# Kernel tuning notes

Measured on AMD Instinct MI355X. Metric: run time of the kernel, lower is better.

Reference implementation:

```python
import jax, jax.numpy as jnp
import numpy as np
from math import factorial

# ---------------- real Wigner-3j coefficients (l <= 2) ----------------

def _w3j_c(l1, l2, l3, m1, m2, m3):
    if m1 + m2 + m3 != 0:
        return 0.0
    f = factorial
    pref = ((-1.0) ** (l1 - l2 - m3)) * np.sqrt(
        f(l1 + l2 - l3) * f(l1 - l2 + l3) * f(-l1 + l2 + l3) / f(l1 + l2 + l3 + 1)
        * f(l1 + m1) * f(l1 - m1) * f(l2 + m2) * f(l2 - m2) * f(l3 + m3) * f(l3 - m3))
    s = 0.0
    for t in range(0, l1 + l2 - l3 + 1):
        ds = [t, l3 - l2 + t + m1, l3 - l1 + t - m2, l1 + l2 - l3 - t, l1 - t - m1, l2 - t + m2]
        if min(ds) < 0:
            continue
        den = 1
        for d in ds:
            den *= f(d)
        s += ((-1.0) ** t) / den
    return pref * s

def _u_real(l):
    # complex->real spherical-harmonic change of basis (rows: mu=-l..l, cols: m=-l..l)
    U = np.zeros((2 * l + 1, 2 * l + 1), dtype=np.complex128)
    U[l, l] = 1.0
    for m in range(1, l + 1):
        U[l + m, l + m] = ((-1) ** m) / np.sqrt(2)
        U[l + m, l - m] = 1.0 / np.sqrt(2)
        U[l - m, l - m] = 1j / np.sqrt(2)
        U[l - m, l + m] = -1j * ((-1) ** m) / np.sqrt(2)
    return U

def _real_w3j(l1, l2, l3):
    W = np.zeros((2 * l1 + 1, 2 * l2 + 1, 2 * l3 + 1), dtype=np.complex128)
    for a, m1 in enumerate(range(-l1, l1 + 1)):
        for b, m2 in enumerate(range(-l2, l2 + 1)):
            for c, m3 in enumerate(range(-l3, l3 + 1)):
                W[a, b, c] = _w3j_c(l1, l2, l3, m1, m2, m3)
    C = np.einsum('am,bn,co,mno->abc', _u_real(l1), _u_real(l2), _u_real(l3), W)
    C = C.real + C.imag  # each entry is purely real or purely imaginary
    n = np.linalg.norm(C)
    if n > 0:
        C = C / n
    return jnp.asarray(C, dtype=jnp.float32)

W3J = {(l1, l2, l3): _real_w3j(l1, l2, l3)
       for l1 in range(3) for l2 in range(3) for l3 in range(3)
       if abs(l1 - l2) <= l3 <= l1 + l2}

SH_OFF = [0, 1, 4]
RELU_GAIN = float(np.sqrt(2.0))  # normalize2mom gain for ReLU

# ---------------- building blocks ----------------

def tp_instructions(in_ls):
    # input irrep blocks have parity (-1)**l (0e,1o,2e); sh = 0e+1o+2e; out = 0e+1o+2e
    ins = []
    for i1, l1 in enumerate(in_ls):
        for l2 in range(3):
            for l3 in range(3):
                if abs(l1 - l2) <= l3 <= l1 + l2 and ((-1) ** (l1 + l2)) == (-1) ** l3:
                    ins.append((i1, l1, l2, l3))
    return ins

def sh_l2(d):
    # component-normalized real spherical harmonics of unit vectors, l=0..2
    x, y, z = d[:, 0], d[:, 1], d[:, 2]
    s3, s15, s5 = np.sqrt(3.0), np.sqrt(15.0), np.sqrt(5.0)
    sh0 = jnp.ones_like(x)[:, None]
    sh1 = jnp.stack([s3 * y, s3 * z, s3 * x], axis=1)
    sh2 = jnp.stack([s15 * x * y, s15 * y * z, (s5 / 2) * (3 * z * z - 1.0),
                     s15 * x * z, (s15 / 2) * (x * x - y * y)], axis=1)
    return jnp.concatenate([sh0, sh1, sh2], axis=1)

def radial_basis(d, num=11, start=0.0, end=8.0):
    values = jnp.linspace(start, end, num)
    step = values[1] - values[0]
    diff = (d[:, None] - values) / step
    return jnp.exp(-(diff * diff)) / 1.12  # e3nn soft_one_hot_linspace 'gaussian'

def radial_net(rb, w1, w2):
    h = jax.nn.relu(rb @ (w1 / np.sqrt(w1.shape[0]))) * RELU_GAIN
    return h @ (w2 / np.sqrt(w2.shape[0]))

def equiv_conv(pos, x, src, dst, rw1, rw2, in_ls, mul_in, C):
    E = src.shape[0]
    vec = pos[src] - pos[dst]                      # (E,3)
    dist = jnp.sqrt(jnp.sum(vec * vec, axis=1))    # (E,)
    w = radial_net(radial_basis(dist), rw1, rw2)   # (E, weight_numel)
    dirs = vec / jnp.maximum(dist, 1e-12)[:, None]
    sh = sh_l2(dirs)                               # (E,9)
    xd = x[dst]                                    # edge gather
    ins = tp_instructions(in_ls)
    fan = {0: 0, 1: 0, 2: 0}
    for (_, l1, l2, l3) in ins:
        fan[l3] += mul_in
    in_off = np.cumsum([0] + [mul_in * (2 * l + 1) for l in in_ls])
    out = [jnp.zeros((E, C, 2 * l3 + 1), x.dtype) for l3 in range(3)]
    woff = 0
    for (i1, l1, l2, l3) in ins:
        x1 = xd[:, in_off[i1]:in_off[i1 + 1]].reshape(E, mul_in, 2 * l1 + 1)
        shb = sh[:, SH_OFF[l2]:SH_OFF[l2] + 2 * l2 + 1]
        wi = w[:, woff:woff + mul_in * C].reshape(E, mul_in, C)
        woff += mul_in * C
        alpha = np.sqrt(2 * l3 + 1) / np.sqrt(fan[l3])
        out[l3] = out[l3] + alpha * jnp.einsum('eui,ej,euw,ijk->ewk', x1, shb, wi, W3J[(l1, l2, l3)])
    msg = jnp.concatenate([o.reshape(E, -1) for o in out], axis=1)
    return jax.ops.segment_sum(msg, src, num_segments=pos.shape[0])  # scatter_add onto src

def self_interaction(x, W, mul_in):
    # x: mul_in x (0e+1o+2e); W: (3, mul_in, mul_out)
    outs, off = [], 0
    for l in range(3):
        d = 2 * l + 1
        b = x[:, off:off + mul_in * d].reshape(-1, mul_in, d)
        off += mul_in * d
        outs.append((jnp.einsum('nui,uw->nwi', b, W[l]) / np.sqrt(mul_in)).reshape(x.shape[0], -1))
    return jnp.concatenate(outs, axis=1)

def pointwise_nonlin(x, b, mul):
    outs, off = [], 0
    for l in range(3):
        d = 2 * l + 1
        blk = x[:, off:off + mul * d]
        off += mul * d
        if l == 0:
            outs.append(jax.nn.softplus(blk + b[0]))
        else:
            v = blk.reshape(-1, mul, d)
            gate = jax.nn.softplus(jnp.sqrt(jnp.sum(v * v, axis=2) + 1e-24) + b[l])
            outs.append((v * gate[:, :, None]).reshape(x.shape[0], -1))
    return jnp.concatenate(outs, axis=1)

def pointwise_norm(x):
    return x / (jnp.linalg.norm(x, axis=1, keepdims=True) + 1e-6)

def backbone(pos, features, edge_index, si0_w, c1_rw1, c1_rw2, si1_w, nl1_b,
             c2_rw1, c2_rw2, si2_w, nl2_b, c3_rw1, c3_rw2, si3_w, nl3_b, fsi_w):
    src, dst = edge_index[0], edge_index[1]
    x = features @ si0_w / np.sqrt(features.shape[1])          # 64x0e -> 128x0e
    x = equiv_conv(pos, x, src, dst, c1_rw1, c1_rw2, [0], 128, 128)
    x = pointwise_norm(x)
    x = self_interaction(x, si1_w, 128)
    x = pointwise_nonlin(x, nl1_b, 128)
    x = equiv_conv(pos, x, src, dst, c2_rw1, c2_rw2, [0, 1, 2], 128, 64)
    x = pointwise_norm(x)
    x = self_interaction(x, si2_w, 64)
    x = pointwise_nonlin(x, nl2_b, 64)
    x = equiv_conv(pos, x, src, dst, c3_rw1, c3_rw2, [0, 1, 2], 64, 32)
    x = pointwise_norm(x)
    x = self_interaction(x, si3_w, 32)
    x = pointwise_nonlin(x, nl3_b, 32)
    x = self_interaction(x, fsi_w, 32)
    return x[:, :32]  # scalar (0e) part

# ---------------- harness ----------------

N_NODES, N_EDGES, FEAT = 512, 2048, 64

def setup_inputs() -> dict:
    key = jax.random.key(0)
    ks = jax.random.split(key, 20)
    src = jax.random.randint(ks[0], (N_EDGES,), 0, N_NODES)
    # avoid self-loops (zero-length edges are degenerate for normalize/grad)
    dst = (src + 1 + jax.random.randint(ks[1], (N_EDGES,), 0, N_NODES - 1)) % N_NODES
    edge_index = jnp.stack([src, dst]).astype(jnp.int64)
    rn = lambda k, s: jax.random.normal(k, s, dtype=jnp.float32)
    return {
        'pos': rn(ks[2], (N_NODES, 3)),
        'features': rn(ks[3], (N_NODES, FEAT)),
        'edge_index': edge_index,
        'si0_w': rn(ks[4], (FEAT, 128)),
        'c1_rw1': rn(ks[5], (11, 12)), 'c1_rw2': rn(ks[6], (12, 3 * 128 * 128)),
        'si1_w': rn(ks[7], (3, 128, 128)), 'nl1_b': jnp.zeros((3,), jnp.float32),
        'c2_rw1': rn(ks[8], (11, 12)), 'c2_rw2': rn(ks[9], (12, 11 * 128 * 64)),
        'si2_w': rn(ks[10], (3, 64, 64)), 'nl2_b': jnp.zeros((3,), jnp.float32),
        'c3_rw1': rn(ks[11], (11, 12)), 'c3_rw2': rn(ks[12], (12, 11 * 64 * 32)),
        'si3_w': rn(ks[13], (3, 32, 32)), 'nl3_b': jnp.zeros((3,), jnp.float32),
        'fsi_w': rn(ks[14], (3, 32, 32)),
    }

def reference(pos, features, edge_index, si0_w, c1_rw1, c1_rw2, si1_w, nl1_b,
              c2_rw1, c2_rw2, si2_w, nl2_b, c3_rw1, c3_rw2, si3_w, nl3_b, fsi_w):
    return backbone(pos, features, edge_index, si0_w, c1_rw1, c1_rw2, si1_w, nl1_b,
                    c2_rw1, c2_rw2, si2_w, nl2_b, c3_rw1, c3_rw2, si3_w, nl3_b, fsi_w)
```

## Files before the change

kernel.cpp:

```cpp
#include <hip/hip_runtime.h>
#include <cmath>
#include <cstdint>

#define NNODES 512
#define NEDGES 2048

typedef _Float16 half2v __attribute__((ext_vector_type(2)));

#define OFF_W3J   0
#define OFF_SH    512
#define OFF_H1    (OFF_SH + NEDGES*9)
#define OFF_H2    (OFF_H1 + NEDGES*6)
#define OFF_H3    (OFF_H2 + NEDGES*6)
#define OFF_W2P1  (OFF_H3 + NEDGES*6)
#define OFF_W2P2  (OFF_W2P1 + 6*49152)
#define OFF_W2P3  (OFF_W2P2 + 6*90112)
#define OFF_XH    (OFF_W2P3 + 6*22528)
#define OFF_XB    (OFF_XH + NNODES*576)
#define OFF_MSGA  (OFF_XB + NNODES*1152)
#define OFF_CNT   (OFF_MSGA + NEDGES*576)
#define OFF_COFF  (OFF_CNT + 512)
#define OFF_LIST  (OFF_COFF + 1024)
#define OFF_RANK  (OFF_LIST + 2048)
#define OFF_MSGB  (OFF_RANK + 2048)
#define WS_NEED_SPLIT ((size_t)(OFF_MSGB + NEDGES*576) * 4)

__device__ __forceinline__ unsigned int packh2f(float a, float b){
  half2v h; h.x=(_Float16)a; h.y=(_Float16)b;
  return __builtin_bit_cast(unsigned int, h);
}
__device__ __forceinline__ half2v u2h2(unsigned int u){ return __builtin_bit_cast(half2v, u); }
__device__ __forceinline__ float dot2f(unsigned int a, unsigned int b, float c){
#if __has_builtin(__builtin_amdgcn_fdot2)
  return __builtin_amdgcn_fdot2(u2h2(a), u2h2(b), c, false);
#else
  half2v ha=u2h2(a), hb=u2h2(b);
  return c + (float)ha.x*(float)hb.x + (float)ha.y*(float)hb.y;
#endif
}
__device__ __forceinline__ unsigned int pk2(float a, float b){
#if __has_builtin(__builtin_amdgcn_cvt_pkrtz)
  auto h=__builtin_amdgcn_cvt_pkrtz(a,b);
  return __builtin_bit_cast(unsigned int,h);
#else
  return packh2f(a,b);
#endif
}
__device__ __forceinline__ unsigned short f2h(float f){
  _Float16 h=(_Float16)f; return __builtin_bit_cast(unsigned short,h);
}
__device__ __forceinline__ float softplusf(float v){ return fmaxf(v,0.f)+log1pf(expf(-fabsf(v))); }

__device__ double dfact(int n){ double f=1.0; for(int i=2;i<=n;++i) f*=(double)i; return f; }

__device__ double w3j_c_dev(int l1,int l2,int l3,int m1,int m2,int m3){
  if (m1+m2+m3 != 0) return 0.0;
  int p = l1 - l2 - m3;
  double sign = (((p%2)+2)%2) ? -1.0 : 1.0;
  double pref = sign*sqrt(dfact(l1+l2-l3)*dfact(l1-l2+l3)*dfact(-l1+l2+l3)/dfact(l1+l2+l3+1)
              *dfact(l1+m1)*dfact(l1-m1)*dfact(l2+m2)*dfact(l2-m2)*dfact(l3+m3)*dfact(l3-m3));
  double s=0.0;
  for (int t=0;t<=l1+l2-l3;++t){
    int d0=t, d1v=l3-l2+t+m1, d2v=l3-l1+t-m2, d3v=l1+l2-l3-t, d4=l1-t-m1, d5=l2-t+m2;
    if (d0<0||d1v<0||d2v<0||d3v<0||d4<0||d5<0) continue;
    double den=dfact(d0)*dfact(d1v)*dfact(d2v)*dfact(d3v)*dfact(d4)*dfact(d5);
    s += ((t&1)?-1.0:1.0)/den;
  }
  return pref*s;
}

__device__ void u_real_dev(int l, double Ur[5][5], double Ui[5][5]){
  for(int a=0;a<5;++a)for(int b=0;b<5;++b){Ur[a][b]=0.0;Ui[a][b]=0.0;}
  Ur[l][l]=1.0;
  double inv2 = 1.0/sqrt(2.0);
  for(int m=1;m<=l;++m){
    double sgn = (m&1)?-1.0:1.0;
    Ur[l+m][l+m] = sgn*inv2;
    Ur[l+m][l-m] = inv2;
    Ui[l-m][l-m] = inv2;
    Ui[l-m][l+m] = -sgn*inv2;
  }
}

__global__ void w3j_kernel(float* __restrict__ out){
  const int L1[11]={0,0,0,1,1,1,1,2,2,2,2};
  const int L2[11]={0,1,2,0,1,1,2,0,1,2,2};
  const int L3[11]={0,1,2,1,0,2,1,2,1,0,2};
  const int OFF[11]={0,1,10,35,44,53,98,143,168,213,238};
  int t = blockIdx.x;
  int tid = threadIdx.x;
  int l1=L1[t], l2=L2[t], l3=L3[t];
  int d1=2*l1+1, d2=2*l2+1, d3=2*l3+1;
  int sz=d1*d2*d3;
  __shared__ double Wt[125];
  __shared__ double U1r[5][5],U1i[5][5],U2r[5][5],U2i[5][5],U3r[5][5],U3i[5][5];
  __shared__ double Cv[125];
  __shared__ double red[128];
  for(int idx=tid; idx<sz; idx+=128){
    int a=idx/(d2*d3), rem=idx%(d2*d3), b=rem/d3, c=rem%d3;
    Wt[idx]=w3j_c_dev(l1,l2,l3,a-l1,b-l2,c-l3);
  }
  if(tid==0) u_real_dev(l1,U1r,U1i);
  if(tid==1) u_real_dev(l2,U2r,U2i);
  if(tid==2) u_real_dev(l3,U3r,U3i);
  __syncthreads();
  for(int idx=tid; idx<sz; idx+=128){
    int a=idx/(d2*d3), rem=idx%(d2*d3), b=rem/d3, c=rem%d3;
    double cr=0.0, ci=0.0;
    for(int m=0;m<d1;++m)for(int n=0;n<d2;++n){
// ... 124 lines not shown
  int i=col>>7, w=col&127;
  int d3=2*i+1;
  float alpha=sqrtf((float)(2*i+1))*(1.f/sqrtf(128.f));
  int e0=blockIdx.x*2;
  #pragma unroll
  for(int s=0;s<2;++s){
    int e=e0+s;
    int n=dstp[e];
    const unsigned int* vp=V+((size_t)n*384+col)*6;
    float G=0.f;
    #pragma unroll
    for(int r2=0;r2<6;++r2) G=dot2f(h1[(size_t)e*6+r2], vp[r2], G);
    int base=(i==0)?0:((i==1)?128:512);
    for(int k=0;k<d3;++k){
      float B=0.f;
      for(int j=0;j<d3;++j) B += shb[(size_t)e*9+i*i+j]*w3j[W3O[i]+j*d3+k];
      m16[(size_t)e*1152 + base + w*d3 + k]=f2h(G*B*alpha);
    }
  }
}

__global__ __launch_bounds__(256) void csr_rank_kernel(const int* __restrict__ src,
    int* __restrict__ cnt, int* __restrict__ rankA){
  __shared__ int s_src[NEDGES];
  int tid=threadIdx.x;
  int4* s4=(int4*)s_src;
  const int4* g4=(const int4*)src;
  for(int i=tid;i<NEDGES/4;i+=256) s4[i]=g4[i];
  __syncthreads();
  int e=blockIdx.x*256+tid;
  int s=s_src[e];
  int lt=0, tot=0;
  for(int b=0;b<NEDGES/4;b+=8){
    int4 v[8];
    #pragma unroll
    for(int k=0;k<8;++k) v[k]=s4[b+k];
    #pragma unroll
    for(int k=0;k<8;++k){
      int j0=4*(b+k);
      tot += ((v[k].x==s)?1:0)+((v[k].y==s)?1:0)+((v[k].z==s)?1:0)+((v[k].w==s)?1:0);
      lt  += ((v[k].x==s&&j0<e)?1:0)+((v[k].y==s&&j0+1<e)?1:0)+((v[k].z==s&&j0+2<e)?1:0)+((v[k].w==s&&j0+3<e)?1:0);
    }
  }
  rankA[e]=lt;
  if(lt==tot-1) cnt[s]=tot;
}

__global__ void csr_scan_kernel(const int* __restrict__ cnt, int* __restrict__ coff){
  __shared__ int s[NNODES];
  int tid=threadIdx.x;
  s[tid]=cnt[tid];
  __syncthreads();
  for(int d=1;d<NNODES;d<<=1){
    int v=(tid>=d)?s[tid-d]:0;
    __syncthreads();
    s[tid]+=v;
    __syncthreads();
  }
  coff[tid+1]=s[tid];
  if(tid==0) coff[0]=0;
}

__global__ void csr_scatter_kernel(const int* __restrict__ src, const int* __restrict__ coff,
    const int* __restrict__ rankA, int* __restrict__ list){
  int e=blockIdx.x*256+threadIdx.x;
  int s=src[e];
  list[coff[s]+rankA[e]]=e;
}

__global__ void si0_kernel(const float* __restrict__ feat, const float* __restrict__ w,
                           unsigned int* __restrict__ xh){
  __shared__ float s_f[64];
  __shared__ unsigned short s_v[128];
  int n=blockIdx.x, tid=threadIdx.x;
  if(tid<64) s_f[tid]=feat[n*64+tid];
  __syncthreads();
  float acc=0.f;
  for(int u=0;u<64;++u) acc += s_f[u]*w[u*128+tid];
  s_v[tid]=f2h(acc*0.125f);
  __syncthreads();
  if(tid<64) xh[(size_t)n*64+tid]=((unsigned int)s_v[2*tid+1]<<16)|s_v[2*tid];
}

struct CInstr { int l1,l2,l3,woff,w3off; float alpha; };
struct LayerArg { CInstr ins[3][4]; int cnt[3]; int gOf[8]; int rank[8]; int nxg[3]; };

template<int MUL,int C,int EB,int NL,int USPLIT,int D3,int L1v>
__device__ __forceinline__ void instr_body(
  const unsigned int* __restrict__ W2h, int nW, int woff,
  const unsigned int (&hreg)[EB][6],
  const uint4* s_xp4, const float* sB,
  float (&acc)[EB][D3], int ubase, int uOff2, int w)
{
  constexpr int D1=2*L1v+1;
  constexpr int MULZ=MUL/USPLIT;
  constexpr int MZ2=MULZ/2;
  constexpr int UC=256/C;
  constexpr int CHZ=MUL/(UC*USPLIT);
  constexpr int CB=(L1v==0)?0:((L1v==1)?MZ2:4*MZ2);
  static_assert(EB==4,"EB must be 4");
  static_assert(CHZ>=2 && (CHZ&1)==0,"CHZ even");
  const unsigned int* Wp = W2h + (size_t)woff + (size_t)ubase*C + w;
  float a2[EB][D1];
  #pragma unroll
  for(int e=0;e<EB;++e){
    #pragma unroll
    for(int i=0;i<D1;++i) a2[e][i]=0.f;
  }
  #pragma unroll 2
  for(int u2=0;u2<CHZ/2;++u2){
    unsigned int wv0[6],wv1[6];
    #pragma unroll
    for(int r=0;r<6;++r){
      wv0[r]=Wp[(size_t)r*nW + (size_t)(2*u2)*C];
      wv1[r]=Wp[(size_t)r*nW + (size_t)(2*u2+1)*C];
    }
    unsigned int wi2[EB];
    #pragma unroll
    for(int e=0;e<EB;++e){
      float w0=0.f,w1=0.f;
      #pragma unroll
      for(int r=0;r<6;++r){ w0=dot2f(hreg[e][r],wv0[r],w0); w1=dot2f(hreg[e][r],wv1[r],w1); }
      wi2[e]=pk2(w0,w1);
    }
    #pragma unroll
    for(int i=0;i<D1;++i){
      uint4 xv = s_xp4[CB + i*MZ2 + uOff2 + u2];
      a2[0][i]=dot2f(wi2[0],xv.x,a2[0][i]);
      a2[1][i]=dot2f(wi2[1],xv.y,a2[1][i]);
      a2[2][i]=dot2f(wi2[2],xv.z,a2[2][i]);
      a2[3][i]=dot2f(wi2[3],xv.w,a2[3][i]);
    }
  }
  #pragma unroll
  for(int e=0;e<EB;++e){
    #pragma unroll
    for(int k=0;k<D3;++k){
      float s=0.f;
      #pragma unroll
      for(int i=0;i<D1;++i) s += a2[e][i]*sB[e*25+i*5+k];
      acc[e][k]+=s;
    }
  }
}

template<int MUL,int C,int EB,int NL,int USPLIT,int D3,int NINS>
__device__ __forceinline__ void conv_main(
  const unsigned int* __restrict__ W2h, int nW,
  const unsigned int (&hreg)[EB][6],
  const uint4* s_xp4, const float* s_B, float* s_red, unsigned short* s_msg,
  unsigned int* __restrict__ msg, const LayerArg& la, int g, int e0,
  int w, int uc, int ubase, int uOff2)
{
  constexpr int UC=256/C;
  const int tid=threadIdx.x;
  float acc[EB][D3];
  #pragma unroll
  for(int e=0;e<EB;++e){
    #pragma unroll
    for(int k=0;k<D3;++k) acc[e][k]=0.f;
  }
  #pragma unroll
  for(int ii=0;ii<NINS;++ii){
    const int l1v=la.ins[g][ii].l1;
    const int woff=la.ins[g][ii].woff;
    switch(l1v){
      case 0: instr_body<MUL,C,EB,NL,USPLIT,D3,0>(W2h,nW,woff,hreg,s_xp4,s_B+ii*EB*25,acc,ubase,uOff2,w); break;
      case 1: instr_body<MUL,C,EB,NL,USPLIT,D3,1>(W2h,nW,woff,hreg,s_xp4,s_B+ii*EB*25,acc,ubase,uOff2,w); break;
      default: instr_body<MUL,C,EB,NL,USPLIT,D3,2>(W2h,nW,woff,hreg,s_xp4,s_B+ii*EB*25,acc,ubase,uOff2,w); break;
    }
  }
  constexpr int L3v=(D3-1)/2;
  constexpr int base32=(L3v==0)?0:((L3v==1)?C/2:2*C);
  constexpr int seg32=C*D3/2;
  for(int e=0;e<EB;++e){
    #pragma unroll
    for(int k=0;k<D3;++k) s_red[k*256+tid]=acc[e][k];
    __syncthreads();
    if(uc==0){
      #pragma unroll
      for(int k=0;k<D3;++k){
        float s=0.f;
        #pragma unroll
        for(int c2=0;c2<UC;++c2) s+=s_red[k*256+c2*C+w];
        s_msg[(e*C+w)*D3+k]=f2h(s);
      }
    }
    __syncthreads();
  }
  const unsigned int* sm32=(const unsigned int*)s_msg;
  for(int ix=tid; ix<EB*seg32; ix+=256){
    int e=ix/seg32, o=ix-e*seg32;
    msg[(size_t)(e0+e)*(9*C/2) + base32 + o] = sm32[e*seg32+o];
  }
}

template<int MUL,int C,int EB,int NL,int USPLIT>
__global__ __launch_bounds__(256,4) void conv_kernel(
  const unsigned int* __restrict__ xh, const unsigned int* __restrict__ W2h, int nW,
  const unsigned int* __restrict__ hb, const float* __restrict__ shb,
  const int* __restrict__ dstp, const float* __restrict__ w3j,
  unsigned int* __restrict__ msg0, unsigned int* __restrict__ msg1, LayerArg la)
{
  constexpr int MUL2=MUL/2;
  constexpr int MULZ=MUL/USPLIT;
  constexpr int MZ2=MULZ/2;
  constexpr int ROW=(NL==1)?MUL2:9*MUL2;
  constexpr int SROW=(NL==1)?MZ2:9*MZ2;
  constexpr int UC=256/C;
  constexpr int CHZ=MUL/(UC*USPLIT);
  constexpr int NB=NEDGES/EB;
  __shared__ unsigned int s_xp[SROW*EB];
  __shared__ float s_B[4*EB*25];
  __shared__ float s_red[5*256];
  __shared__ unsigned short s_msg[EB*C*5];
  int tid=threadIdx.x;
  int bid=blockIdx.x;
  int xcd=bid&7, slot=bid>>3;
  int g=la.gOf[xcd];
  int idx=slot*la.nxg[g]+la.rank[xcd];
  if(idx>=NB*USPLIT) return;
  int zz=idx/NB, et=idx-zz*NB;
  int e0=et*EB;
  unsigned int* msg=(zz==0)?msg0:msg1;
  for(int ix=tid; ix<EB*SROW; ix+=256){
    int e=ix/SROW, c=ix-(ix/SROW)*SROW;
    int l1,i,u2l;
    if(NL==1){ l1=0;i=0;u2l=c; }
    else{
      if(c<MZ2){l1=0;i=0;u2l=c;}
      else if(c<4*MZ2){int t=c-MZ2;i=t/MZ2;u2l=t-i*MZ2;l1=1;}
      else{int t=c-4*MZ2;i=t/MZ2;u2l=t-i*MZ2;l1=2;}
    }
    int gb=(l1==0)?0:((l1==1)?MUL2:4*MUL2);
    int dn=dstp[e0+e];
    s_xp[c*EB+e]=xh[(size_t)dn*ROW + gb + i*MUL2 + zz*MZ2 + u2l];
  }
  int nIns=la.cnt[g];
  for(int ix=tid; ix<nIns*EB*25; ix+=256){
    int ii=ix/(EB*25); int rem=ix%(EB*25); int e=rem/25; int q=rem%25;
    int i=q/5,k=q%5;
    CInstr I=la.ins[g][ii];
    int d1=2*I.l1+1,d2=2*I.l2+1,d3v=2*I.l3+1;
    float v=0.f;
    if(i<d1&&k<d3v){
      int sho=I.l2*I.l2;
      for(int j=0;j<d2;++j) v+=shb[(size_t)(e0+e)*9+sho+j]*w3j[I.w3off+(i*d2+j)*d3v+k];
      v*=I.alpha;
    }
    s_B[(ii*EB+e)*25+q]=v;
  }
  __syncthreads();
  int w=tid%C, uc=tid/C;
  int ubase=zz*MULZ+uc*CHZ;
  int uOff2=uc*(CHZ/2);
  unsigned int hreg[EB][6];
  #pragma unroll
  for(int e=0;e<EB;++e){
    #pragma unroll
    for(int r=0;r<6;++r) hreg[e][r]=hb[(size_t)(e0+e)*6+r];
  }
  const uint4* s_xp4=(const uint4*)s_xp;
  if(NL==1){
    if(g==0)      conv_main<MUL,C,EB,NL,USPLIT,1,1>(W2h,nW,hreg,s_xp4,s_B,s_red,s_msg,msg,la,g,e0,w,uc,ubase,uOff2);
    else if(g==1) conv_main<MUL,C,EB,NL,USPLIT,3,1>(W2h,nW,hreg,s_xp4,s_B,s_red,s_msg,msg,la,g,e0,w,uc,ubase,uOff2);
    else          conv_main<MUL,C,EB,NL,USPLIT,5,1>(W2h,nW,hreg,s_xp4,s_B,s_red,s_msg,msg,la,g,e0,w,uc,ubase,uOff2);
  }else{
    if(g==0)      conv_main<MUL,C,EB,NL,USPLIT,1,3>(W2h,nW,hreg,s_xp4,s_B,s_red,s_msg,msg,la,g,e0,w,uc,ubase,uOff2);
    else if(g==1) conv_main<MUL,C,EB,NL,USPLIT,3,4>(W2h,nW,hreg,s_xp4,s_B,s_red,s_msg,msg,la,g,e0,w,uc,ubase,uOff2);
    else          conv_main<MUL,C,EB,NL,USPLIT,5,4>(W2h,nW,hreg,s_xp4,s_B,s_red,s_msg,msg,la,g,e0,w,uc,ubase,uOff2);
  }
}

__global__ void aggregate_kernel(const unsigned int* __restrict__ msg0,
                                 const unsigned int* __restrict__ msg1,
                                 const int* __restrict__ coff, const int* __restrict__ list,
                                 float* __restrict__ xout, int W32){
  int n=blockIdx.x;
  int b=coff[n], en=coff[n+1];
  for(int c32=threadIdx.x;c32<W32;c32+=blockDim.x){
    float a0=0.f,a1=0.f;
    for(int j=b;j<en;++j){
      size_t o=(size_t)list[j]*W32+c32;
      half2v p=u2h2(msg0[o]); a0+=(float)p.x; a1+=(float)p.y;
      if(msg1){ half2v q=u2h2(msg1[o]); a0+=(float)q.x; a1+=(float)q.y; }
    }
    xout[(size_t)n*(2*W32)+2*c32]=a0;
    xout[(size_t)n*(2*W32)+2*c32+1]=a1;
  }
}

template<int MUL>
__global__ void post_kernel(const float* __restrict__ xin, const float* __restrict__ siw,
                            const float* __restrict__ nlb, unsigned int* __restrict__ xh){
  constexpr int ROW=9*MUL/2;
  __shared__ float s_in[MUL*9];
  __shared__ unsigned short s_out[MUL*9];
  __shared__ float red[256];
  int n=blockIdx.x, tid=threadIdx.x;
  float ss=0.f;
  for(int c=tid;c<MUL*9;c+=256){ float v=xin[(size_t)n*MUL*9+c]; s_in[c]=v; ss+=v*v; }
  red[tid]=ss; __syncthreads();
  for(int d=128;d>0;d>>=1){ if(tid<d) red[tid]+=red[tid+d]; __syncthreads(); }
  float scale=1.f/(sqrtf(red[0])+1e-6f);
  const float inv=scale/sqrtf((float)MUL);
  float b0=nlb[0], b1=nlb[1], b2=nlb[2];
  for(int p=tid;p<3*MUL;p+=256){
    int l=p/MUL, wo=p%MUL;
    if(l==0){
      const float* Wl=siw;
      float a=0.f;
      for(int u=0;u<MUL;++u) a+=s_in[u]*Wl[(size_t)u*MUL+wo];
      s_out[wo]=f2h(softplusf(a*inv+b0));
    } else if(l==1){
      const float* Wl=siw+(size_t)MUL*MUL;
      float v0=0.f,v1=0.f,v2=0.f;
      for(int u=0;u<MUL;++u){
        float wv=Wl[(size_t)u*MUL+wo];
        int bi=MUL+u*3;
        v0+=s_in[bi]*wv; v1+=s_in[bi+1]*wv; v2+=s_in[bi+2]*wv;
      }
      v0*=inv; v1*=inv; v2*=inv;
      float gate=softplusf(sqrtf(v0*v0+v1*v1+v2*v2+1e-24f)+b1);
      int ob=MUL+wo*3;
      s_out[ob]=f2h(v0*gate); s_out[ob+1]=f2h(v1*gate); s_out[ob+2]=f2h(v2*gate);
    } else {
      const float* Wl=siw+(size_t)2*MUL*MUL;
      float v0=0.f,v1=0.f,v2=0.f,v3=0.f,v4=0.f;
      for(int u=0;u<MUL;++u){
        float wv=Wl[(size_t)u*MUL+wo];
        int bi=4*MUL+u*5;
        v0+=s_in[bi]*wv; v1+=s_in[bi+1]*wv; v2+=s_in[bi+2]*wv; v3+=s_in[bi+3]*wv; v4+=s_in[bi+4]*wv;
      }
      v0*=inv; v1*=inv; v2*=inv; v3*=inv; v4*=inv;
      float gate=softplusf(sqrtf(v0*v0+v1*v1+v2*v2+v3*v3+v4*v4+1e-24f)+b2);
      int ob=4*MUL+wo*5;
      s_out[ob]=f2h(v0*gate); s_out[ob+1]=f2h(v1*gate); s_out[ob+2]=f2h(v2*gate);
      s_out[ob+3]=f2h(v3*gate); s_out[ob+4]=f2h(v4*gate);
    }
  }
  __syncthreads();
  for(int p=tid;p<ROW;p+=256){
    int l,i,u2;
    if(p<MUL/2){l=0;i=0;u2=p;}
    else if(p<2*MUL){int t=p-MUL/2;i=t/(MUL/2);u2=t%(MUL/2);l=1;}
    else{int t=p-2*MUL;i=t/(MUL/2);u2=t%(MUL/2);l=2;}
    int d=2*l+1, sb=MUL*l*l;
    unsigned short a=s_out[sb+(2*u2)*d+i], bb=s_out[sb+(2*u2+1)*d+i];
    xh[(size_t)n*ROW+p]=((unsigned int)bb<<16)|a;
  }
}

__global__ void final_kernel(const unsigned int* __restrict__ xh, const float* __restrict__ fsi,
                             float* __restrict__ out){
  int gid=blockIdx.x*blockDim.x+threadIdx.x;
  if(gid>=NNODES*32) return;
  int n=gid/32, wo=gid%32;
  float s=0.f;
  for(int u2=0;u2<16;++u2){
    half2v p=u2h2(xh[(size_t)n*144+u2]);
    s += (float)p.x*fsi[(2*u2)*32+wo] + (float)p.y*fsi[(2*u2+1)*32+wo];
  }
  out[gid]=s*(1.f/sqrtf(32.f));
}

static int w3off_of(int l1,int l2,int l3){
  const int L1[11]={0,0,0,1,1,1,1,2,2,2,2};
  const int L2[11]={0,1,2,0,1,1,2,0,1,2,2};
  const int L3[11]={0,1,2,1,0,2,1,2,1,0,2};
  const int OFF[11]={0,1,10,35,44,53,98,143,168,213,238};
  for(int i=0;i<11;++i) if(L1[i]==l1&&L2[i]==l2&&L3[i]==l3) return OFF[i];
  return 0;
}

static void fill_map(LayerArg& la, const int alloc[3]){
  int x=0;
  for(int g=0;g<3;++g){
    la.nxg[g]=alloc[g];
    for(int r=0;r<alloc[g];++r){ la.gOf[x]=g; la.rank[x]=r; ++x; }
  }
}
static int gridS(const int alloc[3], int NBZ){
  int S=0;
  for(int g=0;g<3;++g){ int s=(NBZ+alloc[g]-1)/alloc[g]; if(s>S)S=s; }
  return S;
}

extern "C" void kernel_launch(void* const* d_in, const int* in_sizes, int n_in,
                              void* d_out, int out_size, void* d_ws, size_t ws_size,
                              hipStream_t stream) {
  const float* pos    = (const float*)d_in[0];
  const float* feat   = (const float*)d_in[1];
  const int*   ei     = (const int*)d_in[2];
  const float* si0w   = (const float*)d_in[3];
  const float* c1_rw1 = (const float*)d_in[4];
  const float* c1_rw2 = (const float*)d_in[5];
  const float* si1w   = (const float*)d_in[6];
  const float* nl1b   = (const float*)d_in[7];
  const float* c2_rw1 = (const float*)d_in[8];
  const float* c2_rw2 = (const float*)d_in[9];
  const float* si2w   = (const float*)d_in[10];
  const float* nl2b   = (const float*)d_in[11];
  const float* c3_rw1 = (const float*)d_in[12];
  const float* c3_rw2 = (const float*)d_in[13];
  const float* si3w   = (const float*)d_in[14];
  const float* nl3b   = (const float*)d_in[15];
  const float* fsiw   = (const float*)d_in[16];

  float* ws_f=(float*)d_ws;
  float* w3   = ws_f+OFF_W3J;
  float* sh   = ws_f+OFF_SH;
  unsigned int* h1   = (unsigned int*)(ws_f+OFF_H1);
  unsigned int* h2   = (unsigned int*)(ws_f+OFF_H2);
  unsigned int* h3   = (unsigned int*)(ws_f+OFF_H3);
  unsigned int* w2p1 = (unsigned int*)(ws_f+OFF_W2P1);
  unsigned int* w2p2 = (unsigned int*)(ws_f+OFF_W2P2);
  unsigned int* w2p3 = (unsigned int*)(ws_f+OFF_W2P3);
  unsigned int* xh   = (unsigned int*)(ws_f+OFF_XH);
  float* xb   = ws_f+OFF_XB;
  unsigned int* msgA = (unsigned int*)(ws_f+OFF_MSGA);
  unsigned int* msgB = (unsigned int*)(ws_f+OFF_MSGB);
  unsigned int* V    = msgB;
  int* cnt    = (int*)(ws_f+OFF_CNT);
  int* coff   = (int*)(ws_f+OFF_COFF);
  int* clist  = (int*)(ws_f+OFF_LIST);
  int* rankA  = (int*)(ws_f+OFF_RANK);
  const int* src  = ei;
  const int* dstp = ei+NEDGES;

  const bool split = ws_size >= WS_NEED_SPLIT;
  const int NB = NEDGES/4;

  LayerArg la1{}, la2{}, la3{};
  {
    int step=128*128;
    for(int i=0;i<3;++i){
      CInstr I{0,i,i, i*step, w3off_of(0,i,i), (float)std::sqrt((2.0*i+1.0)/128.0)};
      la1.ins[i][la1.cnt[i]++]=I;
    }
  }
  const int insL[11][3]={{0,0,0},{0,1,1},{0,2,2},{1,0,1},{1,1,0},{1,1,2},{1,2,1},{2,0,2},{2,1,1},{2,2,0},{2,2,2}};
  auto build=[&](LayerArg& la, int mul, int Cc){
    int step=mul*Cc;
    int fan[3]={0,0,0};
    for(int i=0;i<11;++i) fan[insL[i][2]] += mul;
    for(int i=0;i<11;++i){
      int l1v=insL[i][0],l2v=insL[i][1],l3v=insL[i][2];
      CInstr I{l1v,l2v,l3v, i*step, w3off_of(l1v,l2v,l3v), (float)std::sqrt((2.0*l3v+1.0)/(double)fan[l3v])};
      la.ins[l3v][la.cnt[l3v]++]=I;
    }
  };
  build(la2,128,64);
  build(la3,64,32);

  const int alloc1[3]={3,3,2};
  const int alloc23[3]={2,3,3};
  fill_map(la1,alloc1);
  fill_map(la2,alloc23);
  fill_map(la3,alloc23);

  w3j_kernel<<<dim3(11),dim3(128),0,stream>>>(w3);
  edge_prep_kernel<<<dim3(NEDGES/256),dim3(256),0,stream>>>(pos,ei,c1_rw1,c2_rw1,c3_rw1, sh,h1,h2,h3);
  if(split){
    w1pack_kernel<<<dim3((384*768+255)/256),dim3(256),0,stream>>>(c1_rw2,w2p1);
  } else {
    w2pack_kernel<<<dim3((6*49152+255)/256),dim3(256),0,stream>>>(c1_rw2,w2p1,49152);
  }
  w2pack_kernel<<<dim3((6*90112+255)/256),dim3(256),0,stream>>>(c2_rw2,w2p2,90112);
  w2pack_kernel<<<dim3((6*22528+255)/256),dim3(256),0,stream>>>(c3_rw2,w2p3,22528);

  hipMemsetAsync(cnt,0,NNODES*sizeof(int),stream);
  csr_rank_kernel<<<dim3(NEDGES/256),dim3(256),0,stream>>>(src,cnt,rankA);
  csr_scan_kernel<<<dim3(1),dim3(NNODES),0,stream>>>(cnt,coff);
  csr_scatter_kernel<<<dim3(NEDGES/256),dim3(256),0,stream>>>(src,coff,rankA,clist);

  si0_kernel<<<dim3(NNODES),dim3(128),0,stream>>>(feat,si0w,xh);

  if(split){
    vgemm1_kernel<<<dim3(NNODES/4),dim3(384),0,stream>>>(xh,w2p1,V);
    conv1_edge_kernel<<<dim3(NEDGES/2),dim3(384),0,stream>>>(V,h1,sh,dstp,w3,msgA);
    aggregate_kernel<<<dim3(NNODES),dim3(256),0,stream>>>(msgA,(const unsigned int*)nullptr,coff,clist,xb,576);
    post_kernel<128><<<dim3(NNODES),dim3(256),0,stream>>>(xb,si1w,nl1b,xh);
    int S23=gridS(alloc23,NB*2);
    conv_kernel<128,64,4,3,2><<<dim3(8*S23),dim3(256),0,stream>>>(xh,w2p2,11*128*64,h2,sh,dstp,w3,msgA,msgB,la2);
    aggregate_kernel<<<dim3(NNODES),dim3(256),0,stream>>>(msgA,msgB,coff,clist,xb,288);
    post_kernel<64><<<dim3(NNODES),dim3(256),0,stream>>>(xb,si2w,nl2b,xh);
    int S3=gridS(alloc23,NB);
    conv_kernel<64,32,4,3,1><<<dim3(8*S3),dim3(256),0,stream>>>(xh,w2p3,11*64*32,h3,sh,dstp,w3,msgA,msgA,la3);
    aggregate_kernel<<<dim3(NNODES),dim3(256),0,stream>>>(msgA,(const unsigned int*)nullptr,coff,clist,xb,144);
    post_kernel<32><<<dim3(NNODES),dim3(256),0,stream>>>(xb,si3w,nl3b,xh);
  } else {
    int S1=gridS(alloc1,NB), S23=gridS(alloc23,NB);
    conv_kernel<128,128,4,1,1><<<dim3(8*S1),dim3(256),0,stream>>>(xh,w2p1,3*128*128,h1,sh,dstp,w3,msgA,msgA,la1);
    aggregate_kernel<<<dim3(NNODES),dim3(256),0,stream>>>(msgA,(const unsigned int*)nullptr,coff,clist,xb,576);
    post_kernel<128><<<dim3(NNODES),dim3(256),0,stream>>>(xb,si1w,nl1b,xh);
    conv_kernel<128,64,4,3,1><<<dim3(8*S23),dim3(256),0,stream>>>(xh,w2p2,11*128*64,h2,sh,dstp,w3,msgA,msgA,la2);
    aggregate_kernel<<<dim3(NNODES),dim3(256),0,stream>>>(msgA,(const unsigned int*)nullptr,coff,clist,xb,288);
    post_kernel<64><<<dim3(NNODES),dim3(256),0,stream>>>(xb,si2w,nl2b,xh);
    conv_kernel<64,32,4,3,1><<<dim3(8*S23),dim3(256),0,stream>>>(xh,w2p3,11*64*32,h3,sh,dstp,w3,msgA,msgA,la3);
    aggregate_kernel<<<dim3(NNODES),dim3(256),0,stream>>>(msgA,(const unsigned int*)nullptr,coff,clist,xb,144);
    post_kernel<32><<<dim3(NNODES),dim3(256),0,stream>>>(xb,si3w,nl3b,xh);
  }

  final_kernel<<<dim3((NNODES*32+255)/256),dim3(256),0,stream>>>(xh,fsiw,(float*)d_out);
}
```

Before: 335.7 us.

## Compute all output irreps per block in conv and fuse aggregate with post

The conv kernel no longer splits work by output irrep group across XCD-mapped blocks. Each block now runs all 11 (or 3) instructions for its edge tile with compile-time instruction tables and writes the full 9-component message row. This cuts the redundant gathers of node features and spherical-harmonic coefficients across groups, but each block now carries more accumulator registers, so launch bounds drop to 3 waves per SIMD. Separately, the aggregate and post kernels are fused so the summed messages stay in shared memory, which removes the fp32 intermediate buffer round trip and one launch per layer.

```diff
diff --git a/kernel.cpp b/kernel.cpp
--- a/kernel.cpp
+++ b/kernel.cpp
@@ -25,6 +25,13 @@
 #define OFF_MSGB  (OFF_RANK + 2048)
 #define WS_NEED_SPLIT ((size_t)(OFF_MSGB + NEDGES*576) * 4)
 
+constexpr int IL1[11]={0,0,0,1,1,1,1,2,2,2,2};
+constexpr int IL2[11]={0,1,2,0,1,1,2,0,1,2,2};
+constexpr int IL3[11]={0,1,2,1,0,2,1,2,1,0,2};
+constexpr int IW3O[11]={0,1,10,35,44,53,98,143,168,213,238};
+constexpr int IKOFF[3]={0,1,4};
+constexpr int IFANM[3]={3,4,4};
+
 __device__ __forceinline__ unsigned int packh2f(float a, float b){
   half2v h; h.x=(_Float16)a; h.y=(_Float16)b;
   return __builtin_bit_cast(unsigned int, h);
@@ -315,17 +322,18 @@
   if(tid<64) xh[(size_t)n*64+tid]=((unsigned int)s_v[2*tid+1]<<16)|s_v[2*tid];
 }
 
-struct CInstr { int l1,l2,l3,woff,w3off; float alpha; };
-struct LayerArg { CInstr ins[3][4]; int cnt[3]; int gOf[8]; int rank[8]; int nxg[3]; };
-
-template<int MUL,int C,int EB,int NL,int USPLIT,int D3,int L1v>
-__device__ __forceinline__ void instr_body(
-  const unsigned int* __restrict__ W2h, int nW, int woff,
+template<int MUL,int C,int EB,int NL,int USPLIT,int II>
+__device__ __forceinline__ void instr_one(
+  const unsigned int* __restrict__ W2h, int nW,
   const unsigned int (&hreg)[EB][6],
-  const uint4* s_xp4, const float* sB,
-  float (&acc)[EB][D3], int ubase, int uOff2, int w)
+  const uint4* s_xp4, const float* s_B,
+  float (&acc)[EB][9], int ubase, int uOff2, int w)
 {
+  constexpr int L1v = (NL==1)?0:IL1[II];
+  constexpr int L3v = (NL==1)?((II<3)?II:0):IL3[II];
   constexpr int D1=2*L1v+1;
+  constexpr int D3=2*L3v+1;
+  constexpr int KOFF=IKOFF[L3v];
   constexpr int MULZ=MUL/USPLIT;
   constexpr int MZ2=MULZ/2;
   constexpr int UC=256/C;
@@ -333,7 +341,8 @@
   constexpr int CB=(L1v==0)?0:((L1v==1)?MZ2:4*MZ2);
   static_assert(EB==4,"EB must be 4");
   static_assert(CHZ>=2 && (CHZ&1)==0,"CHZ even");
-  const unsigned int* Wp = W2h + (size_t)woff + (size_t)ubase*C + w;
+  const unsigned int* Wp = W2h + (size_t)(II*MUL*C) + (size_t)ubase*C + w;
+  const float* sB = s_B + II*EB*25;
   float a2[EB][D1];
   #pragma unroll
   for(int e=0;e<EB;++e){
@@ -372,68 +381,17 @@
       float s=0.f;
       #pragma unroll
       for(int i=0;i<D1;++i) s += a2[e][i]*sB[e*25+i*5+k];
-      acc[e][k]+=s;
-    }
-  }
-}
-
-template<int MUL,int C,int EB,int NL,int USPLIT,int D3,int NINS>
-__device__ __forceinline__ void conv_main(
-  const unsigned int* __restrict__ W2h, int nW,
-  const unsigned int (&hreg)[EB][6],
-  const uint4* s_xp4, const float* s_B, float* s_red, unsigned short* s_msg,
-  unsigned int* __restrict__ msg, const LayerArg& la, int g, int e0,
-  int w, int uc, int ubase, int uOff2)
-{
-  constexpr int UC=256/C;
-  const int tid=threadIdx.x;
-  float acc[EB][D3];
-  #pragma unroll
-  for(int e=0;e<EB;++e){
-    #pragma unroll
-    for(int k=0;k<D3;++k) acc[e][k]=0.f;
-  }
-  #pragma unroll
-  for(int ii=0;ii<NINS;++ii){
-    const int l1v=la.ins[g][ii].l1;
-    const int woff=la.ins[g][ii].woff;
-    switch(l1v){
-      case 0: instr_body<MUL,C,EB,NL,USPLIT,D3,0>(W2h,nW,woff,hreg,s_xp4,s_B+ii*EB*25,acc,ubase,uOff2,w); break;
-      case 1: instr_body<MUL,C,EB,NL,USPLIT,D3,1>(W2h,nW,woff,hreg,s_xp4,s_B+ii*EB*25,acc,ubase,uOff2,w); break;
-      default: instr_body<MUL,C,EB,NL,USPLIT,D3,2>(W2h,nW,woff,hreg,s_xp4,s_B+ii*EB*25,acc,ubase,uOff2,w); break;
-    }
-  }
-  constexpr int L3v=(D3-1)/2;
-  constexpr int base32=(L3v==0)?0:((L3v==1)?C/2:2*C);
-  constexpr int seg32=C*D3/2;
-  for(int e=0;e<EB;++e){
-    #pragma unroll
-    for(int k=0;k<D3;++k) s_red[k*256+tid]=acc[e][k];
-    __syncthreads();
-    if(uc==0){
-      #pragma unroll
-      for(int k=0;k<D3;++k){
-        float s=0.f;
-        #pragma unroll
-        for(int c2=0;c2<UC;++c2) s+=s_red[k*256+c2*C+w];
-        s_msg[(e*C+w)*D3+k]=f2h(s);
-      }
-    }
-    __syncthreads();
-  }
-  const unsigned int* sm32=(const unsigned int*)s_msg;
-  for(int ix=tid; ix<EB*seg32; ix+=256){
-    int e=ix/seg32, o=ix-e*seg32;
-    msg[(size_t)(e0+e)*(9*C/2) + base32 + o] = sm32[e*seg32+o];
+      acc[e][KOFF+k]+=s;
+    }
   }
 }
 
 template<int MUL,int C,int EB,int NL,int USPLIT>
-__global__ __launch_bounds__(256,4) void conv_kernel(
+__global__ __launch_bounds__(256,3) void conv_kernel(
   const unsigned int* __restrict__ xh, const unsigned int* __restrict__ W2h, int nW,
   const unsigned int* __restrict__ hb, const float* __restrict__ shb,
   const int* __restrict__ dstp, const float* __restrict__ w3j,
-  unsigned int* __restrict__ msg0, unsigned int* __restrict__ msg1, LayerArg la)
+  unsigned int* __restrict__ msg0, unsigned int* __restrict__ msg1)
 {
   constexpr int MUL2=MUL/2;
   constexpr int MULZ=MUL/USPLIT;
@@ -443,21 +401,19 @@
   constexpr int UC=256/C;
   constexpr int CHZ=MUL/(UC*USPLIT);
   constexpr int NB=NEDGES/EB;
+  constexpr int NI=(NL==1)?3:11;
+  constexpr int SEG=9*C/2;
   __shared__ unsigned int s_xp[SROW*EB];
-  __shared__ float s_B[4*EB*25];
-  __shared__ float s_red[5*256];
-  __shared__ unsigned short s_msg[EB*C*5];
+  __shared__ float s_B[NI*EB*25];
+  __shared__ float s_red[9*256];
+  __shared__ unsigned short s_msg[EB*9*C];
   int tid=threadIdx.x;
   int bid=blockIdx.x;
-  int xcd=bid&7, slot=bid>>3;
-  int g=la.gOf[xcd];
-  int idx=slot*la.nxg[g]+la.rank[xcd];
-  if(idx>=NB*USPLIT) return;
-  int zz=idx/NB, et=idx-zz*NB;
+  int zz=bid/NB, et=bid-zz*NB;
   int e0=et*EB;
   unsigned int* msg=(zz==0)?msg0:msg1;
   for(int ix=tid; ix<EB*SROW; ix+=256){
-    int e=ix/SROW, c=ix-(ix/SROW)*SROW;
+    int e=ix/SROW, c=ix-e*SROW;
     int l1,i,u2l;
     if(NL==1){ l1=0;i=0;u2l=c; }
     else{
@@ -469,17 +425,19 @@
     int dn=dstp[e0+e];
     s_xp[c*EB+e]=xh[(size_t)dn*ROW + gb + i*MUL2 + zz*MZ2 + u2l];
   }
-  int nIns=la.cnt[g];
-  for(int ix=tid; ix<nIns*EB*25; ix+=256){
+  for(int ix=tid; ix<NI*EB*25; ix+=256){
     int ii=ix/(EB*25); int rem=ix%(EB*25); int e=rem/25; int q=rem%25;
     int i=q/5,k=q%5;
-    CInstr I=la.ins[g][ii];
-    int d1=2*I.l1+1,d2=2*I.l2+1,d3v=2*I.l3+1;
+    int l1=(NL==1)?0:IL1[ii];
+    int l2=(NL==1)?ii:IL2[ii];
+    int l3=(NL==1)?ii:IL3[ii];
+    int w3o=(NL==1)?((ii==0)?0:((ii==1)?1:10)):IW3O[ii];
+    int d1=2*l1+1,d2=2*l2+1,d3v=2*l3+1;
     float v=0.f;
     if(i<d1&&k<d3v){
-      int sho=I.l2*I.l2;
-      for(int j=0;j<d2;++j) v+=shb[(size_t)(e0+e)*9+sho+j]*w3j[I.w3off+(i*d2+j)*d3v+k];
-      v*=I.alpha;
+      for(int j=0;j<d2;++j) v+=shb[(size_t)(e0+e)*9+l2*l2+j]*w3j[w3o+(i*d2+j)*d3v+k];
+      float fan=(NL==1)?(float)MUL:(float)(IFANM[l3]*MUL);
+      v*=sqrtf((float)(2*l3+1)/fan);
     }
     s_B[(ii*EB+e)*25+q]=v;
   }
@@ -494,45 +452,69 @@
     for(int r=0;r<6;++r) hreg[e][r]=hb[(size_t)(e0+e)*6+r];
   }
   const uint4* s_xp4=(const uint4*)s_xp;
-  if(NL==1){
-    if(g==0)      conv_main<MUL,C,EB,NL,USPLIT,1,1>(W2h,nW,hreg,s_xp4,s_B,s_red,s_msg,msg,la,g,e0,w,uc,ubase,uOff2);
-    else if(g==1) conv_main<MUL,C,EB,NL,USPLIT,3,1>(W2h,nW,hreg,s_xp4,s_B,s_red,s_msg,msg,la,g,e0,w,uc,ubase,uOff2);
-    else          conv_main<MUL,C,EB,NL,USPLIT,5,1>(W2h,nW,hreg,s_xp4,s_B,s_red,s_msg,msg,la,g,e0,w,uc,ubase,uOff2);
-  }else{
-    if(g==0)      conv_main<MUL,C,EB,NL,USPLIT,1,3>(W2h,nW,hreg,s_xp4,s_B,s_red,s_msg,msg,la,g,e0,w,uc,ubase,uOff2);
-    else if(g==1) conv_main<MUL,C,EB,NL,USPLIT,3,4>(W2h,nW,hreg,s_xp4,s_B,s_red,s_msg,msg,la,g,e0,w,uc,ubase,uOff2);
-    else          conv_main<MUL,C,EB,NL,USPLIT,5,4>(W2h,nW,hreg,s_xp4,s_B,s_red,s_msg,msg,la,g,e0,w,uc,ubase,uOff2);
-  }
-}
-
-__global__ void aggregate_kernel(const unsigned int* __restrict__ msg0,
-                                 const unsigned int* __restrict__ msg1,
-                                 const int* __restrict__ coff, const int* __restrict__ list,
-                                 float* __restrict__ xout, int W32){
-  int n=blockIdx.x;
+  float acc[EB][9];
+  #pragma unroll
+  for(int e=0;e<EB;++e){
+    #pragma unroll
+    for(int kk=0;kk<9;++kk) acc[e][kk]=0.f;
+  }
+  instr_one<MUL,C,EB,NL,USPLIT,0>(W2h,nW,hreg,s_xp4,s_B,acc,ubase,uOff2,w);
+  instr_one<MUL,C,EB,NL,USPLIT,1>(W2h,nW,hreg,s_xp4,s_B,acc,ubase,uOff2,w);
+  instr_one<MUL,C,EB,NL,USPLIT,2>(W2h,nW,hreg,s_xp4,s_B,acc,ubase,uOff2,w);
+  if constexpr (NL==3){
+    instr_one<MUL,C,EB,NL,USPLIT,3>(W2h,nW,hreg,s_xp4,s_B,acc,ubase,uOff2,w);
+    instr_one<MUL,C,EB,NL,USPLIT,4>(W2h,nW,hreg,s_xp4,s_B,acc,ubase,uOff2,w);
+    instr_one<MUL,C,EB,NL,USPLIT,5>(W2h,nW,hreg,s_xp4,s_B,acc,ubase,uOff2,w);
+    instr_one<MUL,C,EB,NL,USPLIT,6>(W2h,nW,hreg,s_xp4,s_B,acc,ubase,uOff2,w);
+    instr_one<MUL,C,EB,NL,USPLIT,7>(W2h,nW,hreg,s_xp4,s_B,acc,ubase,uOff2,w);
+    instr_one<MUL,C,EB,NL,USPLIT,8>(W2h,nW,hreg,s_xp4,s_B,acc,ubase,uOff2,w);
+    instr_one<MUL,C,EB,NL,USPLIT,9>(W2h,nW,hreg,s_xp4,s_B,acc,ubase,uOff2,w);
+    instr_one<MUL,C,EB,NL,USPLIT,10>(W2h,nW,hreg,s_xp4,s_B,acc,ubase,uOff2,w);
+  }
+  for(int e=0;e<EB;++e){
+    #pragma unroll
+    for(int kk=0;kk<9;++kk) s_red[kk*256+tid]=acc[e][kk];
+    __syncthreads();
+    for(int kk=uc;kk<9;kk+=UC){
+      float s=0.f;
+      #pragma unroll
+      for(int c2=0;c2<UC;++c2) s+=s_red[kk*256+c2*C+w];
+      int pos=(kk==0)? w : ((kk<4)? (C+w*3+(kk-1)) : (4*C+w*5+(kk-4)));
+      s_msg[e*9*C+pos]=f2h(s);
+    }
+    __syncthreads();
+  }
+  const unsigned int* sm32=(const unsigned int*)s_msg;
+  for(int ix=tid; ix<EB*SEG; ix+=256){
+    int e=ix/SEG, o=ix-e*SEG;
+    msg[(size_t)(e0+e)*SEG + o] = sm32[e*SEG+o];
+  }
+}
+
+template<int MUL>
+__global__ void agg_post_kernel(const unsigned int* __restrict__ msg0,
+                                const unsigned int* __restrict__ msg1,
+                                const int* __restrict__ coff, const int* __restrict__ list,
+                                const float* __restrict__ siw, const float* __restrict__ nlb,
+                                unsigned int* __restrict__ xh){
+  constexpr int W32=MUL*9/2;
+  constexpr int ROW=9*MUL/2;
+  __shared__ float s_in[MUL*9];
+  __shared__ unsigned short s_out[MUL*9];
+  __shared__ float red[256];
+  int n=blockIdx.x, tid=threadIdx.x;
   int b=coff[n], en=coff[n+1];
-  for(int c32=threadIdx.x;c32<W32;c32+=blockDim.x){
+  float ss=0.f;
+  for(int c32=tid;c32<W32;c32+=256){
     float a0=0.f,a1=0.f;
     for(int j=b;j<en;++j){
       size_t o=(size_t)list[j]*W32+c32;
       half2v p=u2h2(msg0[o]); a0+=(float)p.x; a1+=(float)p.y;
       if(msg1){ half2v q=u2h2(msg1[o]); a0+=(float)q.x; a1+=(float)q.y; }
     }
-    xout[(size_t)n*(2*W32)+2*c32]=a0;
-    xout[(size_t)n*(2*W32)+2*c32+1]=a1;
-  }
-}
-
-template<int MUL>
-__global__ void post_kernel(const float* __restrict__ xin, const float* __restrict__ siw,
-                            const float* __restrict__ nlb, unsigned int* __restrict__ xh){
-  constexpr int ROW=9*MUL/2;
-  __shared__ float s_in[MUL*9];
-  __shared__ unsigned short s_out[MUL*9];
-  __shared__ float red[256];
-  int n=blockIdx.x, tid=threadIdx.x;
-  float ss=0.f;
-  for(int c=tid;c<MUL*9;c+=256){ float v=xin[(size_t)n*MUL*9+c]; s_in[c]=v; ss+=v*v; }
+    s_in[2*c32]=a0; s_in[2*c32+1]=a1;
+    ss+=a0*a0+a1*a1;
+  }
   red[tid]=ss; __syncthreads();
   for(int d=128;d>0;d>>=1){ if(tid<d) red[tid]+=red[tid+d]; __syncthreads(); }
   float scale=1.f/(sqrtf(red[0])+1e-6f);
@@ -597,28 +579,6 @@
   out[gid]=s*(1.f/sqrtf(32.f));
 }
 
-static int w3off_of(int l1,int l2,int l3){
-  const int L1[11]={0,0,0,1,1,1,1,2,2,2,2};
-  const int L2[11]={0,1,2,0,1,1,2,0,1,2,2};
-  const int L3[11]={0,1,2,1,0,2,1,2,1,0,2};
-  const int OFF[11]={0,1,10,35,44,53,98,143,168,213,238};
-  for(int i=0;i<11;++i) if(L1[i]==l1&&L2[i]==l2&&L3[i]==l3) return OFF[i];
-  return 0;
-}
-
-static void fill_map(LayerArg& la, const int alloc[3]){
-  int x=0;
-  for(int g=0;g<3;++g){
-    la.nxg[g]=alloc[g];
-    for(int r=0;r<alloc[g];++r){ la.gOf[x]=g; la.rank[x]=r; ++x; }
-  }
-}
-static int gridS(const int alloc[3], int NBZ){
-  int S=0;
-  for(int g=0;g<3;++g){ int s=(NBZ+alloc[g]-1)/alloc[g]; if(s>S)S=s; }
-  return S;
-}
-
 extern "C" void kernel_launch(void* const* d_in, const int* in_sizes, int n_in,
                               void* d_out, int out_size, void* d_ws, size_t ws_size,
                               hipStream_t stream) {
@@ -650,7 +610,6 @@
   unsigned int* w2p2 = (unsigned int*)(ws_f+OFF_W2P2);
   unsigned int* w2p3 = (unsigned int*)(ws_f+OFF_W2P3);
   unsigned int* xh   = (unsigned int*)(ws_f+OFF_XH);
-  float* xb   = ws_f+OFF_XB;
   unsigned int* msgA = (unsigned int*)(ws_f+OFF_MSGA);
   unsigned int* msgB = (unsigned int*)(ws_f+OFF_MSGB);
   unsigned int* V    = msgB;
@@ -664,34 +623,6 @@
   const bool split = ws_size >= WS_NEED_SPLIT;
   const int NB = NEDGES/4;
 
-  LayerArg la1{}, la2{}, la3{};
-  {
-    int step=128*128;
-    for(int i=0;i<3;++i){
-      CInstr I{0,i,i, i*step, w3off_of(0,i,i), (float)std::sqrt((2.0*i+1.0)/128.0)};
-      la1.ins[i][la1.cnt[i]++]=I;
-    }
-  }
-  const int insL[11][3]={{0,0,0},{0,1,1},{0,2,2},{1,0,1},{1,1,0},{1,1,2},{1,2,1},{2,0,2},{2,1,1},{2,2,0},{2,2,2}};
-  auto build=[&](LayerArg& la, int mul, int Cc){
-    int step=mul*Cc;
-    int fan[3]={0,0,0};
-    for(int i=0;i<11;++i) fan[insL[i][2]] += mul;
-    for(int i=0;i<11;++i){
-      int l1v=insL[i][0],l2v=insL[i][1],l3v=insL[i][2];
-      CInstr I{l1v,l2v,l3v, i*step, w3off_of(l1v,l2v,l3v), (float)std::sqrt((2.0*l3v+1.0)/(double)fan[l3v])};
-      la.ins[l3v][la.cnt[l3v]++]=I;
-    }
-  };
-  build(la2,128,64);
-  build(la3,64,32);
-
-  const int alloc1[3]={3,3,2};
-  const int alloc23[3]={2,3,3};
-  fill_map(la1,alloc1);
-  fill_map(la2,alloc23);
-  fill_map(la3,alloc23);
-
   w3j_kernel<<<dim3(11),dim3(128),0,stream>>>(w3);
   edge_prep_kernel<<<dim3(NEDGES/256),dim3(256),0,stream>>>(pos,ei,c1_rw1,c2_rw1,c3_rw1, sh,h1,h2,h3);
   if(split){
@@ -712,27 +643,18 @@
   if(split){
     vgemm1_kernel<<<dim3(NNODES/4),dim3(384),0,stream>>>(xh,w2p1,V);
     conv1_edge_kernel<<<dim3(NEDGES/2),dim3(384),0,stream>>>(V,h1,sh,dstp,w3,msgA);
-    aggregate_kernel<<<dim3(NNODES),dim3(256),0,stream>>>(msgA,(const unsigned int*)nullptr,coff,clist,xb,576);
-    post_kernel<128><<<dim3(NNODES),dim3(256),0,stream>>>(xb,si1w,nl1b,xh);
-    int S23=gridS(alloc23,NB*2);
-    conv_kernel<128,64,4,3,2><<<dim3(8*S23),dim3(256),0,stream>>>(xh,w2p2,11*128*64,h2,sh,dstp,w3,msgA,msgB,la2);
-    aggregate_kernel<<<dim3(NNODES),dim3(256),0,stream>>>(msgA,msgB,coff,clist,xb,288);
-    post_kernel<64><<<dim3(NNODES),dim3(256),0,stream>>>(xb,si2w,nl2b,xh);
-    int S3=gridS(alloc23,NB);
-    conv_kernel<64,32,4,3,1><<<dim3(8*S3),dim3(256),0,stream>>>(xh,w2p3,11*64*32,h3,sh,dstp,w3,msgA,msgA,la3);
-    aggregate_kernel<<<dim3(NNODES),dim3(256),0,stream>>>(msgA,(const unsigned int*)nullptr,coff,clist,xb,144);
-    post_kernel<32><<<dim3(NNODES),dim3(256),0,stream>>>(xb,si3w,nl3b,xh);
+    agg_post_kernel<128><<<dim3(NNODES),dim3(256),0,stream>>>(msgA,(const unsigned int*)nullptr,coff,clist,si1w,nl1b,xh);
+    conv_kernel<128,64,4,3,2><<<dim3(NB*2),dim3(256),0,stream>>>(xh,w2p2,90112,h2,sh,dstp,w3,msgA,msgB);
+    agg_post_kernel<64><<<dim3(NNODES),dim3(256),0,stream>>>(msgA,msgB,coff,clist,si2w,nl2b,xh);
+    conv_kernel<64,32,4,3,1><<<dim3(NB),dim3(256),0,stream>>>(xh,w2p3,22528,h3,sh,dstp,w3,msgA,msgA);
+    agg_post_kernel<32><<<dim3(NNODES),dim3(256),0,stream>>>(msgA,(const unsigned int*)nullptr,coff,clist,si3w,nl3b,xh);
   } else {
-    int S1=gridS(alloc1,NB), S23=gridS(alloc23,NB);
-    conv_kernel<128,128,4,1,1><<<dim3(8*S1),dim3(256),0,stream>>>(xh,w2p1,3*128*128,h1,sh,dstp,w3,msgA,msgA,la1);
-    aggregate_kernel<<<dim3(NNODES),dim3(256),0,stream>>>(msgA,(const unsigned int*)nullptr,coff,clist,xb,576);
-    post_kernel<128><<<dim3(NNODES),dim3(256),0,stream>>>(xb,si1w,nl1b,xh);
-    conv_kernel<128,64,4,3,1><<<dim3(8*S23),dim3(256),0,stream>>>(xh,w2p2,11*128*64,h2,sh,dstp,w3,msgA,msgA,la2);
-    aggregate_kernel<<<dim3(NNODES),dim3(256),0,stream>>>(msgA,(const unsigned int*)nullptr,coff,clist,xb,288);
-    post_kernel<64><<<dim3(NNODES),dim3(256),0,stream>>>(xb,si2w,nl2b,xh);
-    conv_kernel<64,32,4,3,1><<<dim3(8*S23),dim3(256),0,stream>>>(xh,w2p3,11*64*32,h3,sh,dstp,w3,msgA,msgA,la3);
-    aggregate_kernel<<<dim3(NNODES),dim3(256),0,stream>>>(msgA,(const unsigned int*)nullptr,coff,clist,xb,144);
-    post_kernel<32><<<dim3(NNODES),dim3(256),0,stream>>>(xb,si3w,nl3b,xh);
+    conv_kernel<128,128,4,1,1><<<dim3(NB),dim3(256),0,stream>>>(xh,w2p1,49152,h1,sh,dstp,w3,msgA,msgA);
+    agg_post_kernel<128><<<dim3(NNODES),dim3(256),0,stream>>>(msgA,(const unsigned int*)nullptr,coff,clist,si1w,nl1b,xh);
+    conv_kernel<128,64,4,3,1><<<dim3(NB),dim3(256),0,stream>>>(xh,w2p2,90112,h2,sh,dstp,w3,msgA,msgA);
+    agg_post_kernel<64><<<dim3(NNODES),dim3(256),0,stream>>>(msgA,(const unsigned int*)nullptr,coff,clist,si2w,nl2b,xh);
+    conv_kernel<64,32,4,3,1><<<dim3(NB),dim3(256),0,stream>>>(xh,w2p3,22528,h3,sh,dstp,w3,msgA,msgA);
+    agg_post_kernel<32><<<dim3(NNODES),dim3(256),0,stream>>>(msgA,(const unsigned int*)nullptr,coff,clist,si3w,nl3b,xh);
   }
 
   final_kernel<<<dim3((NNODES*32+255)/256),dim3(256),0,stream>>>(xh,fsiw,(float*)d_out);
```

New measurement: 603.1 us. 79.7% more time.
